# Optimization experiments

Measured on AMD Instinct MI355X. Metric: run time of the kernel, lower is better.

## Reference

```python
import jax, jax.numpy as jnp
import numpy as np

B, L, DM = 4, 1024, 1024
DI = int(2.0 * DM)            # d_inner = ssm_ratio * d_model
N = 16                        # d_state
R = int(np.ceil(DM / 16))     # dt_rank = 64
DT_MIN, DT_MAX = 1e-3, 1e-1


def setup_inputs() -> dict:
    key = jax.random.key(0)
    ks = jax.random.split(key, 8)
    s = 0.02
    # dt_proj bias init: inverse-softplus of log-uniform dt in [dt_min, dt_max]
    dt = jnp.exp(jax.random.uniform(ks[5], (DI,)) * (np.log(DT_MAX) - np.log(DT_MIN)) + np.log(DT_MIN))
    dt_bias = dt + jnp.log(-jnp.expm1(-dt))
    # A_log init: log(1..N) tiled per channel (S4D-real init)
    A_logs = jnp.log(jnp.tile(jnp.arange(1, N + 1, dtype=jnp.float32), (DI, 1)))
    return {
        "x": jax.random.normal(ks[0], (B, L, DM), jnp.float32),
        "W_in": jax.random.normal(ks[1], (DM, 2 * DI), jnp.float32) * s,
        "conv_w": jax.random.normal(ks[2], (DI, 1, 3), jnp.float32) * 0.1,
        "conv_b": jnp.zeros((DI,), jnp.float32),
        "W_x": jax.random.normal(ks[3], (DI, R + 2 * N), jnp.float32) * s,
        "W_dt": jax.random.normal(ks[4], (R, DI), jnp.float32) * (R ** -0.5),
        "dt_bias": dt_bias.astype(jnp.float32),
        "A_logs": A_logs,
        "Ds": jnp.ones((DI,), jnp.float32),
        "ln_g": jnp.ones((DI,), jnp.float32),
        "ln_b": jnp.zeros((DI,), jnp.float32),
        "W_out": jax.random.normal(ks[6], (DI, DM), jnp.float32) * s,
        "b_out": jnp.zeros((DM,), jnp.float32),
    }


def reference(x, W_in, conv_w, conv_b, W_x, W_dt, dt_bias, A_logs, Ds, ln_g, ln_b, W_out, b_out):
    di, n = Ds.shape[0], A_logs.shape[1]
    r = W_dt.shape[0]
    # in_proj and gate branch
    xz = x @ W_in                                   # (B,L,2*di)
    xi = xz[..., :di]
    z = jax.nn.silu(xz[..., di:])                   # (B,L,di)
    # depthwise conv over sequence dim (kernel 3, pad 1)
    xc = jnp.swapaxes(xi, 1, 2)                     # (B,di,L)
    xc = jax.lax.conv_general_dilated(
        xc, conv_w, (1,), [(1, 1)],
        dimension_numbers=("NCH", "OIH", "NCH"),
        feature_group_count=di) + conv_b[None, :, None]
    u = jax.nn.silu(jnp.swapaxes(xc, 1, 2))         # (B,L,di)
    # input-dependent dt, B, C
    x_dbl = u @ W_x                                 # (B,L,r+2n)
    dts = x_dbl[..., :r] @ W_dt                     # (B,L,di)
    Bs = x_dbl[..., r:r + n]                        # (B,L,n)
    Cs = x_dbl[..., r + n:]                         # (B,L,n)
    delta = jax.nn.softplus(dts + dt_bias)          # (B,L,di)
    A = -jnp.exp(A_logs)                            # (di,n)

    def step(h, inp):
        dt, ut, bt, ct = inp                        # (B,di),(B,di),(B,n),(B,n)
        h = jnp.exp(dt[..., None] * A) * h + (dt * ut)[..., None] * bt[:, None, :]
        return h, jnp.einsum("bdn,bn->bd", h, ct)

    xs = (jnp.swapaxes(delta, 0, 1), jnp.swapaxes(u, 0, 1),
          jnp.swapaxes(Bs, 0, 1), jnp.swapaxes(Cs, 0, 1))
    h0 = jnp.zeros((x.shape[0], di, n), x.dtype)
    _, ys = jax.lax.scan(step, h0, xs)              # (L,B,di)
    y = jnp.swapaxes(ys, 0, 1) + Ds * u             # skip term D*u
    # LayerNorm over channels
    mu = y.mean(-1, keepdims=True)
    var = ((y - mu) ** 2).mean(-1, keepdims=True)
    y = (y - mu) / jnp.sqrt(var + 1e-5) * ln_g + ln_b
    y = y * z                                       # gating
    v = y.mean(axis=1)                              # pool='mean' over D
    return v @ W_out + b_out                        # (B, out_dim)
```

## Files before the change

kernel.cpp:

```cpp
#include <hip/hip_runtime.h>
#include <math.h>

#define B_ 4
#define L_ 1024
#define DM_ 1024
#define DI_ 2048
#define N_ 16
#define R_ 64
#define BT_ (B_*L_)
#define NX_ 96
#define CH_ 16
#define LC_ (L_/CH_)
#define KC_ 8
#define KCL_ (DI_/KC_)

typedef unsigned short u16;
typedef unsigned int u32;
typedef short bf16x8 __attribute__((ext_vector_type(8)));
typedef u16 u16x8 __attribute__((ext_vector_type(8)));
typedef float f32x4 __attribute__((ext_vector_type(4)));

__device__ __forceinline__ float silu_f(float x) { return x / (1.f + expf(-x)); }
__device__ __forceinline__ float softplus_f(float x) {
  return x > 0.f ? x + log1pf(expf(-x)) : log1pf(expf(x));
}
__device__ __forceinline__ u16 bf16_rne(float f) {
  u32 u = __float_as_uint(f);
  u32 r = (u + 0x7FFFu + ((u >> 16) & 1u)) >> 16;
  return (u16)r;
}
__device__ __forceinline__ float bf16_to_f(u16 h) {
  return __uint_as_float(((u32)h) << 16);
}

__global__ __launch_bounds__(256) void wsplit_kernel(const float* __restrict__ W,
                                                     u16* __restrict__ Th,
                                                     u16* __restrict__ Tl) {
  __shared__ float tile[32][33];
  const int n0 = blockIdx.x * 32;
  const int k0 = blockIdx.y * 32;
  const int t = threadIdx.x;
  {
    int kr = t >> 3, nc = (t & 7) * 4;
    float4 v = *(const float4*)&W[(size_t)(k0 + kr) * (2 * DI_) + n0 + nc];
    tile[kr][nc + 0] = v.x; tile[kr][nc + 1] = v.y;
    tile[kr][nc + 2] = v.z; tile[kr][nc + 3] = v.w;
  }
  __syncthreads();
  {
    int nr = t >> 3, kc = (t & 7) * 4;
    u16 h[4], l[4];
#pragma unroll
    for (int i = 0; i < 4; ++i) {
      float f = tile[kc + i][nr];
      h[i] = bf16_rne(f);
      l[i] = bf16_rne(f - bf16_to_f(h[i]));
    }
    size_t o = (size_t)(n0 + nr) * DM_ + k0 + kc;
    *(ushort4*)&Th[o] = make_ushort4(h[0], h[1], h[2], h[3]);
    *(ushort4*)&Tl[o] = make_ushort4(l[0], l[1], l[2], l[3]);
  }
}

#define SWZ16(r, s) ((r) * 64 + ((((s) ^ (((r) >> 1) & 3))) << 4))

__global__ __launch_bounds__(256) void gemm1_mfma(const float* __restrict__ A,
                                                  const u16* __restrict__ Bh,
                                                  const u16* __restrict__ Bl,
                                                  float* __restrict__ xi,
                                                  float* __restrict__ z) {
  __shared__ u16 Ah_s[128 * 32];
  __shared__ u16 Al_s[128 * 32];
  __shared__ u16 Bh_s[128 * 32];
  __shared__ u16 Bl_s[128 * 32];

  const int tid = threadIdx.x;
  const int m0 = blockIdx.x * 128;
  const int n0 = blockIdx.y * 128;
  const int wv = tid >> 6;
  const int lane = tid & 63;
  const int wr = wv >> 1, wc = wv & 1;
  const int lrow = lane & 15, lk = lane >> 4;
  const int ra = tid >> 1;
  const int hf = tid & 1;

  f32x4 acc[4][4];
#pragma unroll
  for (int i = 0; i < 4; ++i)
#pragma unroll
    for (int j = 0; j < 4; ++j) acc[i][j] = (f32x4){0.f, 0.f, 0.f, 0.f};

  float af[16];
  uint4 bh0, bh1, bl0, bl1;

  {
    const float* ap = &A[(size_t)(m0 + ra) * DM_ + hf * 16];
    float4 a0 = *(const float4*)(ap + 0);
    float4 a1 = *(const float4*)(ap + 4);
    float4 a2 = *(const float4*)(ap + 8);
    float4 a3 = *(const float4*)(ap + 12);
    af[0]=a0.x; af[1]=a0.y; af[2]=a0.z; af[3]=a0.w;
    af[4]=a1.x; af[5]=a1.y; af[6]=a1.z; af[7]=a1.w;
    af[8]=a2.x; af[9]=a2.y; af[10]=a2.z; af[11]=a2.w;
    af[12]=a3.x; af[13]=a3.y; af[14]=a3.z; af[15]=a3.w;
    const u16* bhp = &Bh[(size_t)(n0 + ra) * DM_ + hf * 16];
    const u16* blp = &Bl[(size_t)(n0 + ra) * DM_ + hf * 16];
    bh0 = *(const uint4*)(bhp + 0);
    bh1 = *(const uint4*)(bhp + 8);
    bl0 = *(const uint4*)(blp + 0);
    bl1 = *(const uint4*)(blp + 8);
  }

  for (int kk = 0; kk < DM_ / 32; ++kk) {
    __syncthreads();
    {
      u16x8 hv0, hv1, lv0, lv1;
#pragma unroll
      for (int i = 0; i < 8; ++i) {
        u16 h = bf16_rne(af[i]);
        hv0[i] = h;
        lv0[i] = bf16_rne(af[i] - bf16_to_f(h));
      }
#pragma unroll
      for (int i = 0; i < 8; ++i) {
        u16 h = bf16_rne(af[8 + i]);
        hv1[i] = h;
        lv1[i] = bf16_rne(af[8 + i] - bf16_to_f(h));
      }
      int s0 = hf * 2;
      *(u16x8*)((char*)Ah_s + SWZ16(ra, s0)) = hv0;
      *(u16x8*)((char*)Ah_s + SWZ16(ra, s0 + 1)) = hv1;
      *(u16x8*)((char*)Al_s + SWZ16(ra, s0)) = lv0;
      *(u16x8*)((char*)Al_s + SWZ16(ra, s0 + 1)) = lv1;
      *(uint4*)((char*)Bh_s + SWZ16(ra, s0)) = bh0;
      *(uint4*)((char*)Bh_s + SWZ16(ra, s0 + 1)) = bh1;
      *(uint4*)((char*)Bl_s + SWZ16(ra, s0)) = bl0;
      *(uint4*)((char*)Bl_s + SWZ16(ra, s0 + 1)) = bl1;
    }
    __syncthreads();

    if (kk + 1 < DM_ / 32) {
      int k0n = (kk + 1) * 32;
      const float* ap = &A[(size_t)(m0 + ra) * DM_ + k0n + hf * 16];
      float4 a0 = *(const float4*)(ap + 0);
      float4 a1 = *(const float4*)(ap + 4);
      float4 a2 = *(const float4*)(ap + 8);
      float4 a3 = *(const float4*)(ap + 12);
      af[0]=a0.x; af[1]=a0.y; af[2]=a0.z; af[3]=a0.w;
      af[4]=a1.x; af[5]=a1.y; af[6]=a1.z; af[7]=a1.w;
      af[8]=a2.x; af[9]=a2.y; af[10]=a2.z; af[11]=a2.w;
      af[12]=a3.x; af[13]=a3.y; af[14]=a3.z; af[15]=a3.w;
      const u16* bhp = &Bh[(size_t)(n0 + ra) * DM_ + k0n + hf * 16];
      const u16* blp = &Bl[(size_t)(n0 + ra) * DM_ + k0n + hf * 16];
      bh0 = *(const uint4*)(bhp + 0);
      bh1 = *(const uint4*)(bhp + 8);
      bl0 = *(const uint4*)(blp + 0);
      bl1 = *(const uint4*)(blp + 8);
    }

    bf16x8 a_h[4], a_l[4], b_h[4], b_l[4];
#pragma unroll
    for (int mi = 0; mi < 4; ++mi) {
      int r = wr * 64 + mi * 16 + lrow;
      a_h[mi] = *(const bf16x8*)((const char*)Ah_s + SWZ16(r, lk));
      a_l[mi] = *(const bf16x8*)((const char*)Al_s + SWZ16(r, lk));
    }
#pragma unroll
    for (int ni = 0; ni < 4; ++ni) {
      int r = wc * 64 + ni * 16 + lrow;
      b_h[ni] = *(const bf16x8*)((const char*)Bh_s + SWZ16(r, lk));
      b_l[ni] = *(const bf16x8*)((const char*)Bl_s + SWZ16(r, lk));
    }
#pragma unroll
    for (int mi = 0; mi < 4; ++mi)
#pragma unroll
      for (int ni = 0; ni < 4; ++ni) {
        acc[mi][ni] = __builtin_amdgcn_mfma_f32_16x16x32_bf16(a_h[mi], b_h[ni], acc[mi][ni], 0, 0, 0);
        acc[mi][ni] = __builtin_amdgcn_mfma_f32_16x16x32_bf16(a_h[mi], b_l[ni], acc[mi][ni], 0, 0, 0);
        acc[mi][ni] = __builtin_amdgcn_mfma_f32_16x16x32_bf16(a_l[mi], b_h[ni], acc[mi][ni], 0, 0, 0);
      }
  }

  const bool is_z = (n0 >= DI_);
#pragma unroll
  for (int mi = 0; mi < 4; ++mi) {
#pragma unroll
    for (int ni = 0; ni < 4; ++ni) {
      int mrow = m0 + wr * 64 + mi * 16 + (lane >> 4) * 4;
      int ncol = n0 + wc * 64 + ni * 16 + (lane & 15);
#pragma unroll
      for (int rg = 0; rg < 4; ++rg) {
        float v = acc[mi][ni][rg];
        int m = mrow + rg;
        if (!is_z) {
          xi[(size_t)m * DI_ + ncol] = v;
        } else {
          z[(size_t)m * DI_ + (ncol - DI_)] = silu_f(v);
        }
      }
    }
  }
}

__global__ __launch_bounds__(256) void conv_silu_kernel(const float* __restrict__ xi,
                                                        const float* __restrict__ cw,
                                                        const float* __restrict__ cb,
                                                        float* __restrict__ u) {
  int idx = blockIdx.x * 256 + threadIdx.x;
  int d = idx & (DI_ - 1);
  int t = (idx >> 11) & (L_ - 1);
  float w0 = cw[d * 3 + 0], w1 = cw[d * 3 + 1], w2 = cw[d * 3 + 2];
  float acc = cb[d] + w1 * xi[idx];
  if (t > 0) acc += w0 * xi[idx - DI_];
  if (t < L_ - 1) acc += w2 * xi[idx + DI_];
  u[idx] = silu_f(acc);
}

__global__ __launch_bounds__(256) void wxsplit_kernel(const float* __restrict__ Wx,
                                                      u16* __restrict__ Th,
                                                      u16* __restrict__ Tl) {
  int gid = blockIdx.x * 256 + threadIdx.x;
  int n = gid >> 11;
  int k = gid & (DI_ - 1);
  float f = Wx[(size_t)k * NX_ + n];
  u16 h = bf16_rne(f);
  Th[gid] = h;
  Tl[gid] = bf16_rne(f - bf16_to_f(h));
}

__global__ __launch_bounds__(256) void xdbl_mfma(const float* __restrict__ U,
                                                 const u16* __restrict__ Wh,
                                                 const u16* __restrict__ Wl,
                                                 float* __restrict__ Pt) {
  __shared__ u16 Uh_s[128 * 32];
  __shared__ u16 Ul_s[128 * 32];
  __shared__ u16 Wh_s[96 * 32];
  __shared__ u16 Wl_s[96 * 32];

  const int tid = threadIdx.x;
  const int m0 = blockIdx.x * 128;
  const int kc = blockIdx.y;
  const int wv = tid >> 6;
  const int lane = tid & 63;
  const int lrow = lane & 15, lk = lane >> 4;
  const int ra = tid >> 1;
  const int hf = tid & 1;

  f32x4 acc[2][6];
#pragma unroll
  for (int i = 0; i < 2; ++i)
#pragma unroll
    for (int j = 0; j < 6; ++j) acc[i][j] = (f32x4){0.f, 0.f, 0.f, 0.f};

  float af[16];
  uint4 wh_r[3], wl_r[3];
  int wc_row[3], wc_slot[3], wc_buf[3];

  {
    int k0 = kc * KCL_;
    const float* up = &U[(size_t)(m0 + ra) * DI_ + k0 + hf * 16];
    float4 a0 = *(const float4*)(up + 0);
    float4 a1 = *(const float4*)(up + 4);
    float4 a2 = *(const float4*)(up + 8);
    float4 a3 = *(const float4*)(up + 12);
    af[0]=a0.x; af[1]=a0.y; af[2]=a0.z; af[3]=a0.w;
    af[4]=a1.x; af[5]=a1.y; af[6]=a1.z; af[7]=a1.w;
    af[8]=a2.x; af[9]=a2.y; af[10]=a2.z; af[11]=a2.w;
    af[12]=a3.x; af[13]=a3.y; af[14]=a3.z; af[15]=a3.w;
#pragma unroll
    for (int i = 0; i < 3; ++i) {
      int c = tid + 256 * i;
      int buf = c >= 384;
      int cc = c & 383;
      int row = cc >> 2, slot = cc & 3;
      wc_buf[i] = buf; wc_row[i] = row; wc_slot[i] = slot;
      const u16* src = (buf ? Wl : Wh) + (size_t)row * DI_ + k0 + slot * 8;
      uint4 v = *(const uint4*)src;
      if (buf) wl_r[i] = v; else wh_r[i] = v;
    }
  }

  for (int kk = 0; kk < KCL_ / 32; ++kk) {
    __syncthreads();
    {
      u16x8 hv0, hv1, lv0, lv1;
#pragma unroll
      for (int i = 0; i < 8; ++i) {
        u16 h = bf16_rne(af[i]);
        hv0[i] = h;
        lv0[i] = bf16_rne(af[i] - bf16_to_f(h));
      }
#pragma unroll
      for (int i = 0; i < 8; ++i) {
        u16 h = bf16_rne(af[8 + i]);
        hv1[i] = h;
        lv1[i] = bf16_rne(af[8 + i] - bf16_to_f(h));
      }
      int s0 = hf * 2;
      *(u16x8*)((char*)Uh_s + SWZ16(ra, s0)) = hv0;
      *(u16x8*)((char*)Uh_s + SWZ16(ra, s0 + 1)) = hv1;
      *(u16x8*)((char*)Ul_s + SWZ16(ra, s0)) = lv0;
      *(u16x8*)((char*)Ul_s + SWZ16(ra, s0 + 1)) = lv1;
#pragma unroll
      for (int i = 0; i < 3; ++i) {
        char* dst = (char*)(wc_buf[i] ? Wl_s : Wh_s) + SWZ16(wc_row[i], wc_slot[i]);
        *(uint4*)dst = wc_buf[i] ? wl_r[i] : wh_r[i];
      }
    }
    __syncthreads();

    if (kk + 1 < KCL_ / 32) {
      int k0 = kc * KCL_ + (kk + 1) * 32;
      const float* up = &U[(size_t)(m0 + ra) * DI_ + k0 + hf * 16];
      float4 a0 = *(const float4*)(up + 0);
      float4 a1 = *(const float4*)(up + 4);
      float4 a2 = *(const float4*)(up + 8);
      float4 a3 = *(const float4*)(up + 12);
      af[0]=a0.x; af[1]=a0.y; af[2]=a0.z; af[3]=a0.w;
      af[4]=a1.x; af[5]=a1.y; af[6]=a1.z; af[7]=a1.w;
      af[8]=a2.x; af[9]=a2.y; af[10]=a2.z; af[11]=a2.w;
      af[12]=a3.x; af[13]=a3.y; af[14]=a3.z; af[15]=a3.w;
#pragma unroll
      for (int i = 0; i < 3; ++i) {
        const u16* src = (wc_buf[i] ? Wl : Wh) + (size_t)wc_row[i] * DI_ + k0 + wc_slot[i] * 8;
        uint4 v = *(const uint4*)src;
        if (wc_buf[i]) wl_r[i] = v; else wh_r[i] = v;
      }
    }

    bf16x8 a_h[2], a_l[2], b_h[6], b_l[6];
#pragma unroll
    for (int mi = 0; mi < 2; ++mi) {
      int r = wv * 32 + mi * 16 + lrow;
      a_h[mi] = *(const bf16x8*)((const char*)Uh_s + SWZ16(r, lk));
      a_l[mi] = *(const bf16x8*)((const char*)Ul_s + SWZ16(r, lk));
    }
#pragma unroll
    for (int ni = 0; ni < 6; ++ni) {
      int r = ni * 16 + lrow;
      b_h[ni] = *(const bf16x8*)((const char*)Wh_s + SWZ16(r, lk));
      b_l[ni] = *(const bf16x8*)((const char*)Wl_s + SWZ16(r, lk));
    }
#pragma unroll
    for (int mi = 0; mi < 2; ++mi)
#pragma unroll
      for (int ni = 0; ni < 6; ++ni) {
        acc[mi][ni] = __builtin_amdgcn_mfma_f32_16x16x32_bf16(a_h[mi], b_h[ni], acc[mi][ni], 0, 0, 0);
        acc[mi][ni] = __builtin_amdgcn_mfma_f32_16x16x32_bf16(a_h[mi], b_l[ni], acc[mi][ni], 0, 0, 0);
        acc[mi][ni] = __builtin_amdgcn_mfma_f32_16x16x32_bf16(a_l[mi], b_h[ni], acc[mi][ni], 0, 0, 0);
      }
  }

#pragma unroll
  for (int mi = 0; mi < 2; ++mi) {
#pragma unroll
    for (int ni = 0; ni < 6; ++ni) {
      int mrow = m0 + wv * 32 + mi * 16 + (lane >> 4) * 4;
      int ncol = ni * 16 + (lane & 15);
#pragma unroll
      for (int rg = 0; rg < 4; ++rg) {
        Pt[((size_t)kc * BT_ + mrow + rg) * NX_ + ncol] = acc[mi][ni][rg];
      }
    }
  }
}

__global__ __launch_bounds__(256) void xdbl_reduce(const float* __restrict__ Pt,
                                                   float* __restrict__ xdbl) {
  int gid = blockIdx.x * 256 + threadIdx.x;
  float s = 0.f;
#pragma unroll
  for (int kc = 0; kc < KC_; ++kc) s += Pt[(size_t)kc * BT_ * NX_ + gid];
  xdbl[gid] = s;
}

__global__ __launch_bounds__(256) void delta_kernel(const float* __restrict__ xdbl,
                                                    const float* __restrict__ Wdt,
                                                    const float* __restrict__ dtb,
                                                    float* __restrict__ delta) {
  __shared__ float xs[8][R_];
  const int m0 = blockIdx.x * 8;
  const int tid = threadIdx.x;
  for (int i = tid; i < 8 * R_; i += 256) {
    int mi = i >> 6, r = i & 63;
    xs[mi][r] = xdbl[(size_t)(m0 + mi) * NX_ + r];
  }
  __syncthreads();
  float acc[8][8];
#pragma unroll
  for (int mi = 0; mi < 8; ++mi)
#pragma unroll
    for (int j = 0; j < 8; ++j) acc[mi][j] = 0.f;

  for (int r = 0; r < R_; ++r) {
    float wd[8];
#pragma unroll
    for (int j = 0; j < 8; ++j) wd[j] = Wdt[(size_t)r * DI_ + tid + j * 256];
#pragma unroll
    for (int mi = 0; mi < 8; ++mi) {
      float xr = xs[mi][r];
#pragma unroll
      for (int j = 0; j < 8; ++j) acc[mi][j] += xr * wd[j];
    }
  }
#pragma unroll
  for (int j = 0; j < 8; ++j) {
    int d = tid + j * 256;
    float bias = dtb[d];
#pragma unroll
    for (int mi = 0; mi < 8; ++mi) {
      delta[(size_t)(m0 + mi) * DI_ + d] = softplus_f(acc[mi][j] + bias);
    }
  }
}

__global__ __launch_bounds__(256) void scanA_kernel(const float* __restrict__ delta,
                                                    const float* __restrict__ u,
                                                    const float* __restrict__ xdbl,
                                                    const float* __restrict__ A_logs,
                                                    float* __restrict__ P,
                                                    float* __restrict__ Q) {
  const int tid = threadIdx.x;
  const int q = tid & 3;
  const int chan = blockIdx.x * 64 + (tid >> 2);
  const int c = blockIdx.y;
  const int b = chan >> 11;
  const int d = chan & (DI_ - 1);
  float Ac[4];
#pragma unroll
  for (int j = 0; j < 4; ++j) Ac[j] = -expf(A_logs[d * N_ + q * 4 + j]);
  const size_t base = (size_t)b * L_ * DI_ + d;
  const float* xd = xdbl + (size_t)b * L_ * NX_;
  float h[4] = {0.f, 0.f, 0.f, 0.f};
  float pr[4] = {1.f, 1.f, 1.f, 1.f};
  const int t0 = c * LC_;
  for (int tt = 0; tt < LC_; ++tt) {
    int t = t0 + tt;
    float dt = delta[base + (size_t)t * DI_];
    float ut = u[base + (size_t)t * DI_];
    float4 Bt = *(const float4*)&xd[t * NX_ + R_ + q * 4];
    float du = dt * ut;
    float e0 = __expf(dt * Ac[0]), e1 = __expf(dt * Ac[1]);
    float e2 = __expf(dt * Ac[2]), e3 = __expf(dt * Ac[3]);
    h[0] = e0 * h[0] + du * Bt.x; pr[0] *= e0;
    h[1] = e1 * h[1] + du * Bt.y; pr[1] *= e1;
    h[2] = e2 * h[2] + du * Bt.z; pr[2] *= e2;
    h[3] = e3 * h[3] + du * Bt.w; pr[3] *= e3;
  }
  size_t idx = ((size_t)chan * CH_ + c) * N_ + q * 4;
  *(float4*)&P[idx] = make_float4(pr[0], pr[1], pr[2], pr[3]);
  *(float4*)&Q[idx] = make_float4(h[0], h[1], h[2], h[3]);
}

__global__ __launch_bounds__(256) void scanB_kernel(const float* __restrict__ P,
                                                    const float* __restrict__ Q,
                                                    float* __restrict__ H0) {
  int gid = blockIdx.x * 256 + threadIdx.x;
  int chan = gid >> 4;
  int n = gid & 15;
  float h = 0.f;
  for (int c = 0; c < CH_; ++c) {
    size_t idx = ((size_t)chan * CH_ + c) * N_ + n;
    H0[idx] = h;
    h = P[idx] * h + Q[idx];
  }
}

__global__ __launch_bounds__(256) void scanC_kernel(const float* __restrict__ delta,
                                                    float* uy,
                                                    const float* __restrict__ xdbl,
                                                    const float* __restrict__ A_logs,
                                                    const float* __restrict__ Ds,
                                                    const float* __restrict__ H0) {
  const int tid = threadIdx.x;
  const int q = tid & 3;
  const int chan = blockIdx.x * 64 + (tid >> 2);
  const int c = blockIdx.y;
  const int b = chan >> 11;
  const int d = chan & (DI_ - 1);
  float Ac[4];
#pragma unroll
  for (int j = 0; j < 4; ++j) Ac[j] = -expf(A_logs[d * N_ + q * 4 + j]);
  const float Dd = Ds[d];
  const size_t base = (size_t)b * L_ * DI_ + d;
  const float* dl = delta + base;
  float* ul = uy + base;
  const float* xd = xdbl + (size_t)b * L_ * NX_;
  float h[4];
  {
    float4 h0 = *(const float4*)&H0[((size_t)chan * CH_ + c) * N_ + q * 4];
    h[0] = h0.x; h[1] = h0.y; h[2] = h0.z; h[3] = h0.w;
  }
  const int t0 = c * LC_;
  for (int tt = 0; tt < LC_; ++tt) {
    int t = t0 + tt;
    float dt = dl[(size_t)t * DI_];
    float ut = ul[(size_t)t * DI_];
    float4 Bt = *(const float4*)&xd[t * NX_ + R_ + q * 4];
    float4 Ct = *(const float4*)&xd[t * NX_ + R_ + N_ + q * 4];
    float du = dt * ut;
    float e0 = __expf(dt * Ac[0]), e1 = __expf(dt * Ac[1]);
    float e2 = __expf(dt * Ac[2]), e3 = __expf(dt * Ac[3]);
    h[0] = e0 * h[0] + du * Bt.x;
    h[1] = e1 * h[1] + du * Bt.y;
    h[2] = e2 * h[2] + du * Bt.z;
    h[3] = e3 * h[3] + du * Bt.w;
    float p = h[0] * Ct.x + h[1] * Ct.y + h[2] * Ct.z + h[3] * Ct.w;
    p += __shfl_xor(p, 1);
    p += __shfl_xor(p, 2);
    if (q == 0) ul[(size_t)t * DI_] = p + Dd * ut;
  }
}

__global__ __launch_bounds__(256) void stats_kernel(const float* __restrict__ y,
                                                    float* __restrict__ mu,
                                                    float* __restrict__ rs) {
  __shared__ float red[4];
  const int row = blockIdx.x;
  const float* yr = y + (size_t)row * DI_;
  const int tid = threadIdx.x;
  float v[8];
  float s = 0.f;
#pragma unroll
  for (int j = 0; j < 8; ++j) { v[j] = yr[tid + j * 256]; s += v[j]; }
#pragma unroll
  for (int o = 1; o < 64; o <<= 1) s += __shfl_xor(s, o);
  if ((tid & 63) == 0) red[tid >> 6] = s;
  __syncthreads();
  float mu_v = (red[0] + red[1] + red[2] + red[3]) * (1.f / DI_);
  float q = 0.f;
#pragma unroll
  for (int j = 0; j < 8; ++j) { float dd = v[j] - mu_v; q += dd * dd; }
#pragma unroll
  for (int o = 1; o < 64; o <<= 1) q += __shfl_xor(q, o);
  __syncthreads();
  if ((tid & 63) == 0) red[tid >> 6] = q;
  __syncthreads();
  if (tid == 0) {
    float var = (red[0] + red[1] + red[2] + red[3]) * (1.f / DI_);
    mu[row] = mu_v;
    rs[row] = rsqrtf(var + 1e-5f);
  }
}

__global__ __launch_bounds__(256) void vacc_kernel(const float* __restrict__ y,
                                                   const float* __restrict__ z,
                                                   const float* __restrict__ mu,
                                                   const float* __restrict__ rs,
                                                   const float* __restrict__ g,
                                                   const float* __restrict__ bb,
                                                   float* __restrict__ v) {
  const int d = blockIdx.x * 256 + threadIdx.x;
  const int t0 = blockIdx.y * 64;
  const int b = blockIdx.z;
  const float gg = g[d], bbv = bb[d];
  float acc = 0.f;
  for (int tt = 0; tt < 64; ++tt) {
    int row = b * L_ + t0 + tt;
    float yv = y[(size_t)row * DI_ + d];
    float zv = z[(size_t)row * DI_ + d];
    acc += ((yv - mu[row]) * rs[row] * gg + bbv) * zv;
  }
  atomicAdd(&v[b * DI_ + d], acc * (1.f / L_));
}

__global__ __launch_bounds__(256) void outinit_kernel(const float* __restrict__ b_out,
                                                      float* __restrict__ out) {
  int i = blockIdx.x * 256 + threadIdx.x;
  out[i] = b_out[i & (DM_ - 1)];
}

__global__ __launch_bounds__(256) void outgemm_kernel(const float* __restrict__ v,
                                                      const float* __restrict__ Wout,
                                                      float* __restrict__ out) {
  const int m = blockIdx.x * 256 + threadIdx.x;
  const int d0 = blockIdx.y * 128;
  float a0 = 0.f, a1 = 0.f, a2 = 0.f, a3 = 0.f;
  for (int dd = 0; dd < 128; ++dd) {
    float w = Wout[(size_t)(d0 + dd) * DM_ + m];
    a0 += v[0 * DI_ + d0 + dd] * w;
    a1 += v[1 * DI_ + d0 + dd] * w;
    a2 += v[2 * DI_ + d0 + dd] * w;
    a3 += v[3 * DI_ + d0 + dd] * w;
  }
  atomicAdd(&out[0 * DM_ + m], a0);
  atomicAdd(&out[1 * DM_ + m], a1);
  atomicAdd(&out[2 * DM_ + m], a2);
  atomicAdd(&out[3 * DM_ + m], a3);
}

extern "C" void kernel_launch(void* const* d_in, const int* in_sizes, int n_in,
                              void* d_out, int out_size, void* d_ws, size_t ws_size,
                              hipStream_t stream) {
  const float* x      = (const float*)d_in[0];
  const float* W_in   = (const float*)d_in[1];
  const float* conv_w = (const float*)d_in[2];
  const float* conv_b = (const float*)d_in[3];
  const float* W_x    = (const float*)d_in[4];
  const float* W_dt   = (const float*)d_in[5];
  const float* dt_bias= (const float*)d_in[6];
  const float* A_logs = (const float*)d_in[7];
  const float* Ds     = (const float*)d_in[8];
  const float* ln_g   = (const float*)d_in[9];
  const float* ln_b   = (const float*)d_in[10];
  const float* W_out  = (const float*)d_in[11];
  const float* b_out  = (const float*)d_in[12];
  float* out = (float*)d_out;

  float* ws = (float*)d_ws;
  const size_t BIG = (size_t)BT_ * DI_;
  float* xi_buf   = ws;
  float* z_buf    = ws + BIG;
  float* u_buf    = ws + 2 * BIG;
  float* xdbl_buf = ws + 3 * BIG;
  float* mu_buf   = xdbl_buf + (size_t)BT_ * NX_;
  float* rs_buf   = mu_buf + BT_;
  float* v_buf    = rs_buf + BT_;
  float* P_buf    = v_buf + (size_t)B_ * DI_;
  float* Q_buf    = P_buf + (size_t)B_ * DI_ * CH_ * N_;
  float* H0_buf   = Q_buf + (size_t)B_ * DI_ * CH_ * N_;

  u16* wt_hi = (u16*)P_buf;
  u16* wt_lo = (u16*)Q_buf;
  u16* wx_hi = (u16*)H0_buf;
  u16* wx_lo = wx_hi + (size_t)NX_ * DI_;
  float* xdbl_part = xi_buf;

  hipMemsetAsync(v_buf, 0, (size_t)B_ * DI_ * sizeof(float), stream);

  wsplit_kernel<<<dim3((2 * DI_) / 32, DM_ / 32), 256, 0, stream>>>(W_in, wt_hi, wt_lo);
  gemm1_mfma<<<dim3(BT_ / 128, (2 * DI_) / 128), 256, 0, stream>>>(x, wt_hi, wt_lo, xi_buf, z_buf);
  conv_silu_kernel<<<(BT_ * DI_) / 256, 256, 0, stream>>>(xi_buf, conv_w, conv_b, u_buf);
  wxsplit_kernel<<<(NX_ * DI_) / 256, 256, 0, stream>>>(W_x, wx_hi, wx_lo);
  xdbl_mfma<<<dim3(BT_ / 128, KC_), 256, 0, stream>>>(u_buf, wx_hi, wx_lo, xdbl_part);
  xdbl_reduce<<<(BT_ * NX_) / 256, 256, 0, stream>>>(xdbl_part, xdbl_buf);
  delta_kernel<<<BT_ / 8, 256, 0, stream>>>(xdbl_buf, W_dt, dt_bias, xi_buf);
  scanA_kernel<<<dim3((B_ * DI_) / 64, CH_), 256, 0, stream>>>(xi_buf, u_buf, xdbl_buf,
                                                               A_logs, P_buf, Q_buf);
  scanB_kernel<<<(B_ * DI_ * N_) / 256, 256, 0, stream>>>(P_buf, Q_buf, H0_buf);
  scanC_kernel<<<dim3((B_ * DI_) / 64, CH_), 256, 0, stream>>>(xi_buf, u_buf, xdbl_buf,
                                                               A_logs, Ds, H0_buf);
  stats_kernel<<<BT_, 256, 0, stream>>>(u_buf, mu_buf, rs_buf);
  vacc_kernel<<<dim3(DI_ / 256, L_ / 64, B_), 256, 0, stream>>>(u_buf, z_buf, mu_buf, rs_buf,
                                                                ln_g, ln_b, v_buf);
  outinit_kernel<<<(B_ * DM_) / 256, 256, 0, stream>>>(b_out, out);
  outgemm_kernel<<<dim3(DM_ / 256, DI_ / 128), 256, 0, stream>>>(v_buf, W_out, out);
}
```

Measured before the change: 358.1 us.

## Pre-split x to bf16 and stream GEMM tiles via global_load_lds

```diff
diff --git a/kernel.cpp b/kernel.cpp
--- a/kernel.cpp
+++ b/kernel.cpp
@@ -32,6 +32,12 @@
 __device__ __forceinline__ float bf16_to_f(u16 h) {
   return __uint_as_float(((u32)h) << 16);
 }
+__device__ __forceinline__ void gload_lds16(const void* g, void* l) {
+  __builtin_amdgcn_global_load_lds((const __attribute__((address_space(1))) void*)g,
+                                   (__attribute__((address_space(3))) void*)l, 16, 0, 0);
+}
+
+#define SWZ16(r, s) ((r) * 64 + ((((s) ^ (((r) >> 1) & 3))) << 4))
 
 __global__ __launch_bounds__(256) void wsplit_kernel(const float* __restrict__ W,
                                                      u16* __restrict__ Th,
@@ -62,27 +68,55 @@
   }
 }
 
-#define SWZ16(r, s) ((r) * 64 + ((((s) ^ (((r) >> 1) & 3))) << 4))
-
-__global__ __launch_bounds__(256) void gemm1_mfma(const float* __restrict__ A,
+__global__ __launch_bounds__(256) void xsplit_kernel(const float* __restrict__ x,
+                                                     u16* __restrict__ xh,
+                                                     u16* __restrict__ xl) {
+  int gid = blockIdx.x * 256 + threadIdx.x;
+  float4 v = *(const float4*)&x[(size_t)gid * 4];
+  ushort4 h, l;
+  h.x = bf16_rne(v.x); l.x = bf16_rne(v.x - bf16_to_f(h.x));
+  h.y = bf16_rne(v.y); l.y = bf16_rne(v.y - bf16_to_f(h.y));
+  h.z = bf16_rne(v.z); l.z = bf16_rne(v.z - bf16_to_f(h.z));
+  h.w = bf16_rne(v.w); l.w = bf16_rne(v.w - bf16_to_f(h.w));
+  *(ushort4*)&xh[(size_t)gid * 4] = h;
+  *(ushort4*)&xl[(size_t)gid * 4] = l;
+}
+
+__global__ __launch_bounds__(512) void gemm1_mfma(const u16* __restrict__ Xh,
+                                                  const u16* __restrict__ Xl,
                                                   const u16* __restrict__ Bh,
                                                   const u16* __restrict__ Bl,
                                                   float* __restrict__ xi,
                                                   float* __restrict__ z) {
-  __shared__ u16 Ah_s[128 * 32];
-  __shared__ u16 Al_s[128 * 32];
-  __shared__ u16 Bh_s[128 * 32];
-  __shared__ u16 Bl_s[128 * 32];
+  __shared__ __align__(16) char lds[49152];
 
   const int tid = threadIdx.x;
   const int m0 = blockIdx.x * 128;
-  const int n0 = blockIdx.y * 128;
+  const int n0 = blockIdx.y * 256;
   const int wv = tid >> 6;
   const int lane = tid & 63;
-  const int wr = wv >> 1, wc = wv & 1;
+  const int wr = wv >> 2, wc = wv & 3;
   const int lrow = lane & 15, lk = lane >> 4;
-  const int ra = tid >> 1;
-  const int hf = tid & 1;
+
+  const u16* gbase[6];
+  int ldsO[6];
+  size_t goff[6];
+#pragma unroll
+  for (int i = 0; i < 6; ++i) {
+    int c = wv * 6 + i;
+    int O = c << 10;
+    int to;
+    const u16* gb;
+    if (O < 8192)       { gb = Xh + (size_t)m0 * DM_; to = O; }
+    else if (O < 16384) { gb = Xl + (size_t)m0 * DM_; to = O - 8192; }
+    else if (O < 32768) { gb = Bh + (size_t)n0 * DM_; to = O - 16384; }
+    else                { gb = Bl + (size_t)n0 * DM_; to = O - 32768; }
+    int r = (to >> 6) + (lane >> 2);
+    int s_src = (lane & 3) ^ ((r >> 1) & 3);
+    gbase[i] = gb;
+    ldsO[i] = O;
+    goff[i] = (size_t)r * DM_ + s_src * 8;
+  }
 
   f32x4 acc[4][4];
 #pragma unroll
@@ -90,86 +124,26 @@
 #pragma unroll
     for (int j = 0; j < 4; ++j) acc[i][j] = (f32x4){0.f, 0.f, 0.f, 0.f};
 
-  float af[16];
-  uint4 bh0, bh1, bl0, bl1;
-
-  {
-    const float* ap = &A[(size_t)(m0 + ra) * DM_ + hf * 16];
-    float4 a0 = *(const float4*)(ap + 0);
-    float4 a1 = *(const float4*)(ap + 4);
-    float4 a2 = *(const float4*)(ap + 8);
-    float4 a3 = *(const float4*)(ap + 12);
-    af[0]=a0.x; af[1]=a0.y; af[2]=a0.z; af[3]=a0.w;
-    af[4]=a1.x; af[5]=a1.y; af[6]=a1.z; af[7]=a1.w;
-    af[8]=a2.x; af[9]=a2.y; af[10]=a2.z; af[11]=a2.w;
-    af[12]=a3.x; af[13]=a3.y; af[14]=a3.z; af[15]=a3.w;
-    const u16* bhp = &Bh[(size_t)(n0 + ra) * DM_ + hf * 16];
-    const u16* blp = &Bl[(size_t)(n0 + ra) * DM_ + hf * 16];
-    bh0 = *(const uint4*)(bhp + 0);
-    bh1 = *(const uint4*)(bhp + 8);
-    bl0 = *(const uint4*)(blp + 0);
-    bl1 = *(const uint4*)(blp + 8);
-  }
-
   for (int kk = 0; kk < DM_ / 32; ++kk) {
+    const int k0 = kk * 32;
+#pragma unroll
+    for (int i = 0; i < 6; ++i) {
+      gload_lds16(gbase[i] + goff[i] + k0, lds + ldsO[i]);
+    }
     __syncthreads();
-    {
-      u16x8 hv0, hv1, lv0, lv1;
-#pragma unroll
-      for (int i = 0; i < 8; ++i) {
-        u16 h = bf16_rne(af[i]);
-        hv0[i] = h;
-        lv0[i] = bf16_rne(af[i] - bf16_to_f(h));
-      }
-#pragma unroll
-      for (int i = 0; i < 8; ++i) {
-        u16 h = bf16_rne(af[8 + i]);
-        hv1[i] = h;
-        lv1[i] = bf16_rne(af[8 + i] - bf16_to_f(h));
-      }
-      int s0 = hf * 2;
-      *(u16x8*)((char*)Ah_s + SWZ16(ra, s0)) = hv0;
-      *(u16x8*)((char*)Ah_s + SWZ16(ra, s0 + 1)) = hv1;
-      *(u16x8*)((char*)Al_s + SWZ16(ra, s0)) = lv0;
-      *(u16x8*)((char*)Al_s + SWZ16(ra, s0 + 1)) = lv1;
-      *(uint4*)((char*)Bh_s + SWZ16(ra, s0)) = bh0;
-      *(uint4*)((char*)Bh_s + SWZ16(ra, s0 + 1)) = bh1;
-      *(uint4*)((char*)Bl_s + SWZ16(ra, s0)) = bl0;
-      *(uint4*)((char*)Bl_s + SWZ16(ra, s0 + 1)) = bl1;
-    }
-    __syncthreads();
-
-    if (kk + 1 < DM_ / 32) {
-      int k0n = (kk + 1) * 32;
-      const float* ap = &A[(size_t)(m0 + ra) * DM_ + k0n + hf * 16];
-      float4 a0 = *(const float4*)(ap + 0);
-      float4 a1 = *(const float4*)(ap + 4);
-      float4 a2 = *(const float4*)(ap + 8);
-      float4 a3 = *(const float4*)(ap + 12);
-      af[0]=a0.x; af[1]=a0.y; af[2]=a0.z; af[3]=a0.w;
-      af[4]=a1.x; af[5]=a1.y; af[6]=a1.z; af[7]=a1.w;
-      af[8]=a2.x; af[9]=a2.y; af[10]=a2.z; af[11]=a2.w;
-      af[12]=a3.x; af[13]=a3.y; af[14]=a3.z; af[15]=a3.w;
-      const u16* bhp = &Bh[(size_t)(n0 + ra) * DM_ + k0n + hf * 16];
-      const u16* blp = &Bl[(size_t)(n0 + ra) * DM_ + k0n + hf * 16];
-      bh0 = *(const uint4*)(bhp + 0);
-      bh1 = *(const uint4*)(bhp + 8);
-      bl0 = *(const uint4*)(blp + 0);
-      bl1 = *(const uint4*)(blp + 8);
-    }
 
     bf16x8 a_h[4], a_l[4], b_h[4], b_l[4];
 #pragma unroll
     for (int mi = 0; mi < 4; ++mi) {
       int r = wr * 64 + mi * 16 + lrow;
-      a_h[mi] = *(const bf16x8*)((const char*)Ah_s + SWZ16(r, lk));
-      a_l[mi] = *(const bf16x8*)((const char*)Al_s + SWZ16(r, lk));
+      a_h[mi] = *(const bf16x8*)(lds + SWZ16(r, lk));
+      a_l[mi] = *(const bf16x8*)(lds + 8192 + SWZ16(r, lk));
     }
 #pragma unroll
     for (int ni = 0; ni < 4; ++ni) {
       int r = wc * 64 + ni * 16 + lrow;
-      b_h[ni] = *(const bf16x8*)((const char*)Bh_s + SWZ16(r, lk));
-      b_l[ni] = *(const bf16x8*)((const char*)Bl_s + SWZ16(r, lk));
+      b_h[ni] = *(const bf16x8*)(lds + 16384 + SWZ16(r, lk));
+      b_l[ni] = *(const bf16x8*)(lds + 32768 + SWZ16(r, lk));
     }
 #pragma unroll
     for (int mi = 0; mi < 4; ++mi)
@@ -179,6 +153,7 @@
         acc[mi][ni] = __builtin_amdgcn_mfma_f32_16x16x32_bf16(a_h[mi], b_l[ni], acc[mi][ni], 0, 0, 0);
         acc[mi][ni] = __builtin_amdgcn_mfma_f32_16x16x32_bf16(a_l[mi], b_h[ni], acc[mi][ni], 0, 0, 0);
       }
+    __syncthreads();
   }
 
   const bool is_z = (n0 >= DI_);
@@ -206,14 +181,33 @@
                                                         const float* __restrict__ cw,
                                                         const float* __restrict__ cb,
                                                         float* __restrict__ u) {
-  int idx = blockIdx.x * 256 + threadIdx.x;
+  int gid = blockIdx.x * 256 + threadIdx.x;
+  int idx = gid * 4;
   int d = idx & (DI_ - 1);
   int t = (idx >> 11) & (L_ - 1);
-  float w0 = cw[d * 3 + 0], w1 = cw[d * 3 + 1], w2 = cw[d * 3 + 2];
-  float acc = cb[d] + w1 * xi[idx];
-  if (t > 0) acc += w0 * xi[idx - DI_];
-  if (t < L_ - 1) acc += w2 * xi[idx + DI_];
-  u[idx] = silu_f(acc);
+  float4 xc = *(const float4*)&xi[idx];
+  float4 xm = make_float4(0.f, 0.f, 0.f, 0.f);
+  float4 xp = make_float4(0.f, 0.f, 0.f, 0.f);
+  if (t > 0) xm = *(const float4*)&xi[idx - DI_];
+  if (t < L_ - 1) xp = *(const float4*)&xi[idx + DI_];
+  float4 o;
+  {
+    float w0 = cw[(d + 0) * 3], w1 = cw[(d + 0) * 3 + 1], w2 = cw[(d + 0) * 3 + 2];
+    o.x = silu_f(cb[d + 0] + w0 * xm.x + w1 * xc.x + w2 * xp.x);
+  }
+  {
+    float w0 = cw[(d + 1) * 3], w1 = cw[(d + 1) * 3 + 1], w2 = cw[(d + 1) * 3 + 2];
+    o.y = silu_f(cb[d + 1] + w0 * xm.y + w1 * xc.y + w2 * xp.y);
+  }
+  {
+    float w0 = cw[(d + 2) * 3], w1 = cw[(d + 2) * 3 + 1], w2 = cw[(d + 2) * 3 + 2];
+    o.z = silu_f(cb[d + 2] + w0 * xm.z + w1 * xc.z + w2 * xp.z);
+  }
+  {
+    float w0 = cw[(d + 3) * 3], w1 = cw[(d + 3) * 3 + 1], w2 = cw[(d + 3) * 3 + 2];
+    o.w = silu_f(cb[d + 3] + w0 * xm.w + w1 * xc.w + w2 * xp.w);
+  }
+  *(float4*)&u[idx] = o;
 }
 
 __global__ __launch_bounds__(256) void wxsplit_kernel(const float* __restrict__ Wx,
@@ -624,13 +618,17 @@
   u16* wt_lo = (u16*)Q_buf;
   u16* wx_hi = (u16*)H0_buf;
   u16* wx_lo = wx_hi + (size_t)NX_ * DI_;
+  u16* xh = (u16*)u_buf;
+  u16* xl = xh + (size_t)BT_ * DM_;
   float* xdbl_part = xi_buf;
 
   hipMemsetAsync(v_buf, 0, (size_t)B_ * DI_ * sizeof(float), stream);
 
   wsplit_kernel<<<dim3((2 * DI_) / 32, DM_ / 32), 256, 0, stream>>>(W_in, wt_hi, wt_lo);
-  gemm1_mfma<<<dim3(BT_ / 128, (2 * DI_) / 128), 256, 0, stream>>>(x, wt_hi, wt_lo, xi_buf, z_buf);
-  conv_silu_kernel<<<(BT_ * DI_) / 256, 256, 0, stream>>>(xi_buf, conv_w, conv_b, u_buf);
+  xsplit_kernel<<<(BT_ * DM_) / 1024, 256, 0, stream>>>(x, xh, xl);
+  gemm1_mfma<<<dim3(BT_ / 128, (2 * DI_) / 256), 512, 0, stream>>>(xh, xl, wt_hi, wt_lo,
+                                                                   xi_buf, z_buf);
+  conv_silu_kernel<<<(BT_ * DI_) / 1024, 256, 0, stream>>>(xi_buf, conv_w, conv_b, u_buf);
   wxsplit_kernel<<<(NX_ * DI_) / 256, 256, 0, stream>>>(W_x, wx_hi, wx_lo);
   xdbl_mfma<<<dim3(BT_ / 128, KC_), 256, 0, stream>>>(u_buf, wx_hi, wx_lo, xdbl_part);
   xdbl_reduce<<<(BT_ * NX_) / 256, 256, 0, stream>>>(xdbl_part, xdbl_buf);
```

After: 334.9 us. 1.07x faster.
